# Optimization experiments

Hardware: AMD Instinct MI355X
Metric: run time of the kernel (lower is better)

Reference implementation:

```python
import jax, jax.numpy as jnp
import numpy as np


def setup_inputs() -> dict:
    key = jax.random.key(0)
    ks = jax.random.split(key, 6)
    N, E, C_in, C_out, C_e = 50000, 800000, 64, 64, 1
    x = jax.random.normal(ks[0], (N, C_in), dtype=jnp.float32)
    edge_index = jax.random.randint(ks[1], (2, E), 0, N, dtype=jnp.int64)
    edge_attr = jax.random.uniform(ks[2], (E, C_e), dtype=jnp.float32)
    W_fc = jax.random.normal(ks[3], (C_out, C_in), dtype=jnp.float32) * (1.0 / np.sqrt(C_in))
    W_edge = jax.random.normal(ks[4], (C_e, C_e), dtype=jnp.float32) * (1.0 / np.sqrt(C_in))
    W_att = jax.random.normal(ks[5], (1, 2 * C_out + C_e), dtype=jnp.float32) * (1.0 / np.sqrt(C_in))
    return {"x": x, "edge_index": edge_index, "edge_attr": edge_attr,
            "W_fc": W_fc, "W_edge": W_edge, "W_att": W_att}


def reference(x, edge_index, edge_attr, W_fc, W_edge, W_att):
    # x: [N, C_in], edge_index: [2, E], edge_attr: [E, C_e]
    row, col = edge_index[0], edge_index[1]
    num_node = x.shape[0]
    xcol = x[col] @ W_fc.T            # [E, C_out] gather + linear
    xrow = x[row] @ W_fc.T            # [E, C_out]
    ed = edge_attr @ W_edge.T         # [E, C_e]
    alpha = jnp.concatenate([xrow, xcol, ed], axis=1) @ W_att.T  # [E, 1]
    alpha = jax.nn.leaky_relu(alpha, negative_slope=0.01)
    # Faithful to source: softmax over singleton dim=1 -> all ones.
    alpha = jax.nn.softmax(alpha, axis=1)
    h = alpha * xcol                  # [E, C_out]
    z = jax.ops.segment_sum(h, row, num_segments=num_node)  # scatter_sum over dst
    return z
```

## Files before the change

kernel.cpp:

```cpp
#include <hip/hip_runtime.h>
#include <hip/hip_bf16.h>


#define BSHIFT 6
#define BNODES 64
#define CAPB 2048
#define CAP 48
#define SPILLCAP 65536
#define MAXNB 1024

__device__ inline unsigned short f2bf(float f) {
    __hip_bfloat16 h = __float2bfloat16(f);
    return *reinterpret_cast<unsigned short*>(&h);
}

__global__ void zero_kernel(int* __restrict__ a, int n) {
    int i = blockIdx.x * blockDim.x + threadIdx.x;
    int s = gridDim.x * blockDim.x;
    for (; i < n; i += s) a[i] = 0;
}

__global__ __launch_bounds__(256) void fc_split(
        const float* __restrict__ x, const float* __restrict__ Wfc,
        unsigned short* __restrict__ y, int N,
        const int* __restrict__ eidx, int2* __restrict__ buckets,
        int* __restrict__ cursor, int* __restrict__ spillcnt, int* __restrict__ spill,
        int E, int NB, int splitB) {
    if ((int)blockIdx.x < splitB) {
        __shared__ int hist[MAXNB];
        __shared__ int bases[MAXNB];
        int chunk = (E + splitB - 1) / splitB;
        int e0 = (int)blockIdx.x * chunk;
        int e1 = e0 + chunk; if (e1 > E) e1 = E;
        for (int i = threadIdx.x; i < NB; i += 256) hist[i] = 0;
        __syncthreads();
        for (int e = e0 + threadIdx.x; e < e1; e += 256)
            atomicAdd(&hist[eidx[e] >> BSHIFT], 1);
        __syncthreads();
        for (int b = threadIdx.x; b < NB; b += 256) {
            int c = hist[b];
            bases[b] = c ? atomicAdd(&cursor[b * 16], c) : 0;
            hist[b] = 0;
        }
        __syncthreads();
        for (int e = e0 + threadIdx.x; e < e1; e += 256) {
            int r = eidx[e];
            int c = eidx[E + e];
            int b = r >> BSHIFT;
            int pos = bases[b] + atomicAdd(&hist[b], 1);
            if (pos < CAPB) {
                buckets[(size_t)b * CAPB + pos] = make_int2(r, c);
            } else {
                int q = atomicAdd(spillcnt, 1);
                if (q < SPILLCAP) { spill[2 * q] = r; spill[2 * q + 1] = c; }
            }
        }
    } else {
        __shared__ float sW[64][68];
        __shared__ float sX[16][64];
        for (int i = threadIdx.x; i < 4096; i += 256) sW[i >> 6][i & 63] = Wfc[i];
        int row0 = ((int)blockIdx.x - splitB) << 4;
        for (int i = threadIdx.x; i < 1024; i += 256) {
            int r = i >> 6, k = i & 63, gr = row0 + r;
            sX[r][k] = (gr < N) ? x[(size_t)gr * 64 + k] : 0.f;
        }
        __syncthreads();
        int co = threadIdx.x & 63;
        int rq = threadIdx.x >> 6;
        const float4* wrow = reinterpret_cast<const float4*>(&sW[co][0]);
        const float4* xr0  = reinterpret_cast<const float4*>(&sX[4 * rq + 0][0]);
        const float4* xr1  = reinterpret_cast<const float4*>(&sX[4 * rq + 1][0]);
        const float4* xr2  = reinterpret_cast<const float4*>(&sX[4 * rq + 2][0]);
        const float4* xr3  = reinterpret_cast<const float4*>(&sX[4 * rq + 3][0]);
        float a0 = 0, a1 = 0, a2 = 0, a3 = 0;
#pragma unroll
        for (int m = 0; m < 16; ++m) {
            float4 w  = wrow[m];
            float4 v0 = xr0[m], v1 = xr1[m], v2 = xr2[m], v3 = xr3[m];
            a0 = fmaf(w.x, v0.x, fmaf(w.y, v0.y, fmaf(w.z, v0.z, fmaf(w.w, v0.w, a0))));
            a1 = fmaf(w.x, v1.x, fmaf(w.y, v1.y, fmaf(w.z, v1.z, fmaf(w.w, v1.w, a1))));
            a2 = fmaf(w.x, v2.x, fmaf(w.y, v2.y, fmaf(w.z, v2.z, fmaf(w.w, v2.w, a2))));
            a3 = fmaf(w.x, v3.x, fmaf(w.y, v3.y, fmaf(w.z, v3.z, fmaf(w.w, v3.w, a3))));
        }
        int g = row0 + 4 * rq;
        if (g + 3 < N) {
            y[(size_t)(g + 0) * 64 + co] = f2bf(a0);
            y[(size_t)(g + 1) * 64 + co] = f2bf(a1);
            y[(size_t)(g + 2) * 64 + co] = f2bf(a2);
            y[(size_t)(g + 3) * 64 + co] = f2bf(a3);
        } else {
            if (g + 0 < N) y[(size_t)(g + 0) * 64 + co] = f2bf(a0);
            if (g + 1 < N) y[(size_t)(g + 1) * 64 + co] = f2bf(a1);
            if (g + 2 < N) y[(size_t)(g + 2) * 64 + co] = f2bf(a2);
        }
    }
}

__device__ inline void acc_bf8(const uint2* yb, int c, int ch4,
                               float& r0, float& r1, float& r2, float& r3) {
    uint2 u = yb[(size_t)c * 16 + ch4];
    r0 += __uint_as_float(u.x << 16);
    r1 += __uint_as_float(u.x & 0xffff0000u);
    r2 += __uint_as_float(u.y << 16);
    r3 += __uint_as_float(u.y & 0xffff0000u);
}
__global__ __launch_bounds__(512) void gatherz2(
        const int2* __restrict__ buckets, const int* __restrict__ cursor,
        const uint2* __restrict__ yb2, float4* __restrict__ z4, int N,
        int* __restrict__ spillcnt, int* __restrict__ spill) {
    __shared__ int cntL[BNODES];
    __shared__ int slotsL[BNODES * CAP];
    int b  = (int)blockIdx.x;
    int lo = b << BSHIFT;
    for (int i = threadIdx.x; i < BNODES; i += 512) cntL[i] = 0;
    __syncthreads();
    int ecnt = cursor[b * 16]; if (ecnt > CAPB) ecnt = CAPB;
    const int2* blist = buckets + (size_t)b * CAPB;
    for (int t = threadIdx.x; t < ecnt; t += 512) {
        int2 ed = blist[t];
        int n = ed.x - lo;
        int slot = atomicAdd(&cntL[n], 1);
        if (slot < CAP) {
            slotsL[n * CAP + slot] = ed.y;
        } else {
            int q = atomicAdd(spillcnt, 1);
            if (q < SPILLCAP) { spill[2 * q] = ed.x; spill[2 * q + 1] = ed.y; }
        }
    }
    __syncthreads();
    int lane = threadIdx.x & 63;
    int wv   = threadIdx.x >> 6;
    int sub  = lane >> 4;
    int ch4  = lane & 15;
    for (int n = wv; n < BNODES; n += 8) {
        int node = lo + n;
        if (node >= N) break;
        int deg = cntL[n]; if (deg > CAP) deg = CAP;
        const int* srow = &slotsL[n * CAP];
        float A0=0,A1=0,A2=0,A3=0, B0=0,B1=0,B2=0,B3=0,
              C0=0,C1=0,C2=0,C3=0, D0=0,D1=0,D2=0,D3=0;
        for (int j = 0; j < deg; j += 16) {
            int j0 = j + sub, j1 = j + 4 + sub, j2 = j + 8 + sub, j3 = j + 12 + sub;
            int c0 = (j0 < deg) ? srow[j0] : -1;
            int c1 = (j1 < deg) ? srow[j1] : -1;
            int c2 = (j2 < deg) ? srow[j2] : -1;
            int c3 = (j3 < deg) ? srow[j3] : -1;
            if (c0 >= 0) acc_bf8(yb2, c0, ch4, A0, A1, A2, A3);
            if (c1 >= 0) acc_bf8(yb2, c1, ch4, B0, B1, B2, B3);
            if (c2 >= 0) acc_bf8(yb2, c2, ch4, C0, C1, C2, C3);
            if (c3 >= 0) acc_bf8(yb2, c3, ch4, D0, D1, D2, D3);
        }
        float r0 = (A0 + B0) + (C0 + D0);
        float r1 = (A1 + B1) + (C1 + D1);
        float r2 = (A2 + B2) + (C2 + D2);
        float r3 = (A3 + B3) + (C3 + D3);
        r0 += __shfl_xor(r0, 16, 64); r0 += __shfl_xor(r0, 32, 64);
        r1 += __shfl_xor(r1, 16, 64); r1 += __shfl_xor(r1, 32, 64);
        r2 += __shfl_xor(r2, 16, 64); r2 += __shfl_xor(r2, 32, 64);
        r3 += __shfl_xor(r3, 16, 64); r3 += __shfl_xor(r3, 32, 64);
        if (lane < 16)
            z4[(size_t)node * 16 + ch4] = make_float4(r0, r1, r2, r3);
    }
}

__global__ void spill_fix(const int* __restrict__ spillcnt, const int* __restrict__ spill,
                          const unsigned short* __restrict__ yb, float* __restrict__ z) {
    int n = *spillcnt;
    if (n > SPILLCAP) n = SPILLCAP;
    int lane = threadIdx.x & 63;
    int g  = (int)((blockIdx.x * blockDim.x + threadIdx.x) >> 6);
    int nG = (int)((gridDim.x * blockDim.x) >> 6);
    for (int i = g; i < n; i += nG) {
        int r = spill[2 * i], c = spill[2 * i + 1];
        unsigned short u = yb[(size_t)c * 64 + lane];
        atomicAdd(&z[(size_t)r * 64 + lane], __uint_as_float(((unsigned)u) << 16));
    }
}

__global__ void fc_kernel(const float* __restrict__ x, const float* __restrict__ Wfc,
                          float* __restrict__ y, int N) {
    __shared__ float sW[64][65];
    __shared__ float sX[4][64];
    for (int i = threadIdx.x; i < 64 * 64; i += 256) sW[i >> 6][i & 63] = Wfc[i];
    int r = threadIdx.x >> 6, co = threadIdx.x & 63;
    int gRow = (blockIdx.x << 2) + r;
    sX[r][co] = (gRow < N) ? x[gRow * 64 + co] : 0.f;
    __syncthreads();
    if (gRow >= N) return;
    float acc = 0.f;
#pragma unroll
    for (int k = 0; k < 64; ++k) acc = fmaf(sX[r][k], sW[co][k], acc);
    y[gRow * 64 + co] = acc;
}
__global__ void scatter_kernel(const int* __restrict__ eidx, const float* __restrict__ y,
                               float* __restrict__ z, int E) {
    int lane = threadIdx.x & 63;
    int g  = (int)((blockIdx.x * blockDim.x + threadIdx.x) >> 6);
    int nG = (int)((gridDim.x * blockDim.x) >> 6);
    for (int e = g; e < E; e += nG) {
        int r = eidx[e], c = eidx[E + e];
        atomicAdd(&z[r * 64 + lane], y[c * 64 + lane]);
    }
}

extern "C" void kernel_launch(void* const* d_in, const int* in_sizes, int n_in,
                              void* d_out, int out_size, void* d_ws, size_t ws_size,
                              hipStream_t stream) {
    const float* x    = (const float*)d_in[0];
    const int*   eidx = (const int*)d_in[1];
    const float* Wfc  = (const float*)d_in[3];
    float*       z    = (float*)d_out;

    int N = in_sizes[0] / 64;
    int E = in_sizes[1] / 2;
    int NB = (N + BNODES - 1) >> BSHIFT;

    char* w = (char*)d_ws;
    size_t off = 0;
    int* cursor   = (int*)(w + off); off += (size_t)NB * 16 * sizeof(int);
    int* spillcnt = (int*)(w + off); off += sizeof(int);
    off = (off + 255) & ~(size_t)255;
    int* spill    = (int*)(w + off); off += (size_t)2 * SPILLCAP * sizeof(int);
    off = (off + 255) & ~(size_t)255;
    int2* buckets = (int2*)(w + off); off += (size_t)NB * CAPB * sizeof(int2);
    off = (off + 255) & ~(size_t)255;
    unsigned short* yb = (unsigned short*)(w + off); off += (size_t)N * 64 * sizeof(unsigned short);

    if (ws_size >= off && NB <= MAXNB) {
        zero_kernel<<<32, 256, 0, stream>>>(cursor, NB * 16 + 1);
        int splitB = 128;
        int fcB = (N + 15) / 16;
        fc_split<<<splitB + fcB, 256, 0, stream>>>(x, Wfc, yb, N, eidx, buckets,
                                                   cursor, spillcnt, spill, E, NB, splitB);
        gatherz2<<<NB, 512, 0, stream>>>(buckets, cursor, (const uint2*)yb,
                                         (float4*)z, N, spillcnt, spill);
        spill_fix<<<64, 256, 0, stream>>>(spillcnt, spill, yb, z);
    } else {
        float* y = (float*)d_ws;
        hipMemsetAsync(d_out, 0, (size_t)out_size * sizeof(float), stream);
        fc_kernel<<<(N + 3) / 4, 256, 0, stream>>>(x, Wfc, y, N);
        scatter_kernel<<<4096, 256, 0, stream>>>(eidx, y, z, E);
    }
}
```

Measured before the change: 60.37 us.

## Pack bucket edges into 32-bit words and fold spill handling into gather

Bucket entries are packed as a 6-bit local node plus 16-bit column in one unsigned, which halves the bucket write and read traffic. The gather kernel reads two entries per load, keeps per-node slot overflow in a shared-memory list, and scans the global spill list itself. This removes the separate spill_fix kernel launch and its float atomics. The edge-split block count is also halved. The fast path now requires N <= 65536, and every gather block rescans the whole spill list, which costs extra if spills are common.

```diff
diff --git a/kernel.cpp b/kernel.cpp
--- a/kernel.cpp
+++ b/kernel.cpp
@@ -6,6 +6,7 @@
 #define BNODES 64
 #define CAPB 2048
 #define CAP 48
+#define OVFCAP 128
 #define SPILLCAP 65536
 #define MAXNB 1024
 
@@ -23,7 +24,7 @@
 __global__ __launch_bounds__(256) void fc_split(
         const float* __restrict__ x, const float* __restrict__ Wfc,
         unsigned short* __restrict__ y, int N,
-        const int* __restrict__ eidx, int2* __restrict__ buckets,
+        const int* __restrict__ eidx, unsigned* __restrict__ buckets,
         int* __restrict__ cursor, int* __restrict__ spillcnt, int* __restrict__ spill,
         int E, int NB, int splitB) {
     if ((int)blockIdx.x < splitB) {
@@ -49,7 +50,8 @@
             int b = r >> BSHIFT;
             int pos = bases[b] + atomicAdd(&hist[b], 1);
             if (pos < CAPB) {
-                buckets[(size_t)b * CAPB + pos] = make_int2(r, c);
+                buckets[(size_t)b * CAPB + pos] =
+                    ((unsigned)(r & (BNODES - 1)) << 16) | (unsigned)c;
             } else {
                 int q = atomicAdd(spillcnt, 1);
                 if (q < SPILLCAP) { spill[2 * q] = r; spill[2 * q + 1] = c; }
@@ -105,29 +107,56 @@
     r3 += __uint_as_float(u.y & 0xffff0000u);
 }
 __global__ __launch_bounds__(512) void gatherz2(
-        const int2* __restrict__ buckets, const int* __restrict__ cursor,
+        const unsigned* __restrict__ buckets, const int* __restrict__ cursor,
         const uint2* __restrict__ yb2, float4* __restrict__ z4, int N,
-        int* __restrict__ spillcnt, int* __restrict__ spill) {
+        const int* __restrict__ spillcnt, const int* __restrict__ spill) {
     __shared__ int cntL[BNODES];
     __shared__ int slotsL[BNODES * CAP];
+    __shared__ int ovfN[OVFCAP], ovfC[OVFCAP], ovfn_sh;
     int b  = (int)blockIdx.x;
     int lo = b << BSHIFT;
     for (int i = threadIdx.x; i < BNODES; i += 512) cntL[i] = 0;
+    if (threadIdx.x == 0) ovfn_sh = 0;
     __syncthreads();
     int ecnt = cursor[b * 16]; if (ecnt > CAPB) ecnt = CAPB;
-    const int2* blist = buckets + (size_t)b * CAPB;
-    for (int t = threadIdx.x; t < ecnt; t += 512) {
-        int2 ed = blist[t];
-        int n = ed.x - lo;
+    const unsigned* blist = buckets + (size_t)b * CAPB;
+    const uint2* blist2 = (const uint2*)blist;
+    int nPairs = ecnt >> 1;
+    for (int p = threadIdx.x; p < nPairs; p += 512) {
+        uint2 ee = blist2[p];
+#pragma unroll
+        for (int h = 0; h < 2; ++h) {
+            unsigned e = h ? ee.y : ee.x;
+            int n = (int)(e >> 16);
+            int c = (int)(e & 0xffffu);
+            int slot = atomicAdd(&cntL[n], 1);
+            if (slot < CAP) slotsL[n * CAP + slot] = c;
+            else { int q = atomicAdd(&ovfn_sh, 1);
+                   if (q < OVFCAP) { ovfN[q] = n; ovfC[q] = c; } }
+        }
+    }
+    if ((ecnt & 1) && threadIdx.x == 0) {
+        unsigned e = blist[ecnt - 1];
+        int n = (int)(e >> 16), c = (int)(e & 0xffffu);
         int slot = atomicAdd(&cntL[n], 1);
-        if (slot < CAP) {
-            slotsL[n * CAP + slot] = ed.y;
-        } else {
-            int q = atomicAdd(spillcnt, 1);
-            if (q < SPILLCAP) { spill[2 * q] = ed.x; spill[2 * q + 1] = ed.y; }
+        if (slot < CAP) slotsL[n * CAP + slot] = c;
+        else { int q = atomicAdd(&ovfn_sh, 1);
+               if (q < OVFCAP) { ovfN[q] = n; ovfC[q] = c; } }
+    }
+    int sc = *spillcnt;
+    if (sc > SPILLCAP) sc = SPILLCAP;
+    for (int i = threadIdx.x; i < sc; i += 512) {
+        int r = spill[2 * i];
+        if ((r >> BSHIFT) == b) {
+            int n = r & (BNODES - 1), c = spill[2 * i + 1];
+            int slot = atomicAdd(&cntL[n], 1);
+            if (slot < CAP) slotsL[n * CAP + slot] = c;
+            else { int q = atomicAdd(&ovfn_sh, 1);
+                   if (q < OVFCAP) { ovfN[q] = n; ovfC[q] = c; } }
         }
     }
     __syncthreads();
+    int on = ovfn_sh; if (on > OVFCAP) on = OVFCAP;
     int lane = threadIdx.x & 63;
     int wv   = threadIdx.x >> 6;
     int sub  = lane >> 4;
@@ -150,6 +179,9 @@
             if (c2 >= 0) acc_bf8(yb2, c2, ch4, C0, C1, C2, C3);
             if (c3 >= 0) acc_bf8(yb2, c3, ch4, D0, D1, D2, D3);
         }
+        for (int k = 0; k < on; ++k)
+            if (ovfN[k] == n && sub == 0)
+                acc_bf8(yb2, ovfC[k], ch4, A0, A1, A2, A3);
         float r0 = (A0 + B0) + (C0 + D0);
         float r1 = (A1 + B1) + (C1 + D1);
         float r2 = (A2 + B2) + (C2 + D2);
@@ -160,20 +192,6 @@
         r3 += __shfl_xor(r3, 16, 64); r3 += __shfl_xor(r3, 32, 64);
         if (lane < 16)
             z4[(size_t)node * 16 + ch4] = make_float4(r0, r1, r2, r3);
-    }
-}
-
-__global__ void spill_fix(const int* __restrict__ spillcnt, const int* __restrict__ spill,
-                          const unsigned short* __restrict__ yb, float* __restrict__ z) {
-    int n = *spillcnt;
-    if (n > SPILLCAP) n = SPILLCAP;
-    int lane = threadIdx.x & 63;
-    int g  = (int)((blockIdx.x * blockDim.x + threadIdx.x) >> 6);
-    int nG = (int)((gridDim.x * blockDim.x) >> 6);
-    for (int i = g; i < n; i += nG) {
-        int r = spill[2 * i], c = spill[2 * i + 1];
-        unsigned short u = yb[(size_t)c * 64 + lane];
-        atomicAdd(&z[(size_t)r * 64 + lane], __uint_as_float(((unsigned)u) << 16));
     }
 }
 
@@ -222,19 +240,18 @@
     off = (off + 255) & ~(size_t)255;
     int* spill    = (int*)(w + off); off += (size_t)2 * SPILLCAP * sizeof(int);
     off = (off + 255) & ~(size_t)255;
-    int2* buckets = (int2*)(w + off); off += (size_t)NB * CAPB * sizeof(int2);
+    unsigned* buckets = (unsigned*)(w + off); off += (size_t)NB * CAPB * sizeof(unsigned);
     off = (off + 255) & ~(size_t)255;
     unsigned short* yb = (unsigned short*)(w + off); off += (size_t)N * 64 * sizeof(unsigned short);
 
-    if (ws_size >= off && NB <= MAXNB) {
+    if (ws_size >= off && NB <= MAXNB && N <= 65536) {
         zero_kernel<<<32, 256, 0, stream>>>(cursor, NB * 16 + 1);
-        int splitB = 128;
+        int splitB = 64;
         int fcB = (N + 15) / 16;
         fc_split<<<splitB + fcB, 256, 0, stream>>>(x, Wfc, yb, N, eidx, buckets,
                                                    cursor, spillcnt, spill, E, NB, splitB);
         gatherz2<<<NB, 512, 0, stream>>>(buckets, cursor, (const uint2*)yb,
                                          (float4*)z, N, spillcnt, spill);
-        spill_fix<<<64, 256, 0, stream>>>(spillcnt, spill, yb, z);
     } else {
         float* y = (float*)d_ws;
         hipMemsetAsync(d_out, 0, (size_t)out_size * sizeof(float), stream);
```

New measurement: 70.04 us. 1.16x slower.
